# Kernel optimization log

Hardware: AMD Instinct MI355X
Metric: run time of the kernel (lower is better)

The kernel has to match this reference:

```python
import jax, jax.numpy as jnp
import numpy as np
from jax import lax

LEAK = 0.2
GN_EPS = 1e-5
K_NEIGH = 16
GROUPS = 4


def knn_idx(coor_k, coor_q, k):
    # coor_k: [B,Nk,3], coor_q: [B,Nq,3] -> [B,Nq,k] indices of k nearest in coor_k
    d = (jnp.sum(coor_q * coor_q, -1, keepdims=True)
         - 2.0 * jnp.einsum('bqc,bkc->bqk', coor_q, coor_k)
         + jnp.sum(coor_k * coor_k, -1)[:, None, :])
    _, idx = lax.top_k(-d, k)
    return idx


def graph_feature(coor_q, x_q, coor_k, x_k, k):
    # coor_*: [B,3,N*]; x_q: [B,C,Nq]; x_k: [B,C,Nk] -> [B,2C,Nq,k]
    idx = knn_idx(lax.stop_gradient(coor_k).transpose(0, 2, 1),
                  lax.stop_gradient(coor_q).transpose(0, 2, 1), k)
    B = x_k.shape[0]
    x_k_t = x_k.transpose(0, 2, 1)                      # [B,Nk,C]
    b_idx = jnp.arange(B)[:, None, None]
    nb = x_k_t[b_idx, idx]                              # [B,Nq,k,C]
    nb = nb.transpose(0, 3, 1, 2)                       # [B,C,Nq,k]
    xq = x_q[:, :, :, None]                             # [B,C,Nq,1]
    return jnp.concatenate([nb - xq, jnp.broadcast_to(xq, nb.shape)], axis=1)


def conv_gn_lrelu_max(f, w, gamma, beta):
    # f: [B,Cin,N,k]; w: [Cout,Cin] -> [B,Cout,N] (max over k)
    y = jnp.einsum('oc,bcnk->bonk', w, f)
    B, C, N, Kk = y.shape
    g = y.reshape(B, GROUPS, C // GROUPS, N, Kk)
    mu = g.mean((2, 3, 4), keepdims=True)
    var = g.var((2, 3, 4), keepdims=True)
    g = (g - mu) * lax.rsqrt(var + GN_EPS)
    y = g.reshape(B, C, N, Kk) * gamma[None, :, None, None] + beta[None, :, None, None]
    y = jnp.where(y >= 0, y, LEAK * y)
    return y.max(axis=-1)


def fps(xyz, n):
    # xyz: [B,N,3] -> [B,n] int32 (furthest point sampling, start at index 0)
    B, N, _ = xyz.shape
    d0 = jnp.sum((xyz - xyz[:, :1]) ** 2, -1)           # dist to point 0
    def body(dist, _):
        idx = jnp.argmax(dist, -1)                       # [B]
        nxt = jnp.take_along_axis(xyz, idx[:, None, None], 1)
        dist = jnp.minimum(dist, jnp.sum((xyz - nxt) ** 2, -1))
        return dist, idx
    _, idxs = lax.scan(body, d0, None, length=n - 1)     # [n-1,B]
    first = jnp.zeros((1, B), idxs.dtype)
    return jnp.concatenate([first, idxs], 0).T           # [B,n]


def fps_downsample(coor, x, n):
    # coor: [B,3,N], x: [B,C,N] -> ([B,3,n], [B,C,n])
    idx = fps(lax.stop_gradient(coor).transpose(0, 2, 1), n)
    comb = jnp.concatenate([coor, x], axis=1)            # [B,3+C,N]
    b_idx = jnp.arange(coor.shape[0])[:, None]
    new = comb.transpose(0, 2, 1)[b_idx, idx].transpose(0, 2, 1)
    return new[:, :3], new[:, 3:]


def setup_inputs() -> dict:
    key = jax.random.key(0)
    ks = jax.random.split(key, 16)
    s = 0.1
    return {
        'x': jax.random.normal(ks[0], (32, 2048, 3), jnp.float32),
        'w_in': jax.random.normal(ks[1], (8, 3), jnp.float32) * s,
        'b_in': jnp.zeros((8,), jnp.float32),
        'w1': jax.random.normal(ks[2], (32, 16), jnp.float32) * s,
        'g1': jnp.ones((32,), jnp.float32), 'be1': jnp.zeros((32,), jnp.float32),
        'w2': jax.random.normal(ks[3], (64, 64), jnp.float32) * s,
        'g2': jnp.ones((64,), jnp.float32), 'be2': jnp.zeros((64,), jnp.float32),
        'w3': jax.random.normal(ks[4], (64, 128), jnp.float32) * s,
        'g3': jnp.ones((64,), jnp.float32), 'be3': jnp.zeros((64,), jnp.float32),
        'w4': jax.random.normal(ks[5], (256, 128), jnp.float32) * s,
        'g4': jnp.ones((256,), jnp.float32), 'be4': jnp.zeros((256,), jnp.float32),
        'num0': 512,
        'num1': 128,
    }


def reference(x, w_in, b_in, w1, g1, be1, w2, g2, be2, w3, g3, be3, w4, g4, be4, num0, num1):
    coor = x.transpose(0, 2, 1)                          # [B,3,N]
    f = jnp.einsum('oc,bcn->bon', w_in, coor) + b_in[None, :, None]  # input_trans
    f = graph_feature(coor, f, coor, f, K_NEIGH)         # [B,16,N,k]
    f = conv_gn_lrelu_max(f, w1, g1, be1)                # [B,32,N]
    coor_q, f_q = fps_downsample(coor, f, num0)
    f = graph_feature(coor_q, f_q, coor, f, K_NEIGH)     # [B,64,num0,k]
    f = conv_gn_lrelu_max(f, w2, g2, be2)                # [B,64,num0]
    coor = coor_q
    f = graph_feature(coor, f, coor, f, K_NEIGH)         # [B,128,num0,k]
    f = conv_gn_lrelu_max(f, w3, g3, be3)                # [B,64,num0]
    coor_q, f_q = fps_downsample(coor, f, num1)
    f = graph_feature(coor_q, f_q, coor, f, K_NEIGH)     # [B,128,num1,k]
    f = conv_gn_lrelu_max(f, w4, g4, be4)                # [B,256,num1]
    coor = coor_q
    return coor.transpose(0, 2, 1), f.transpose(0, 2, 1)  # [B,num1,3], [B,num1,256]
```

## Files before the change

### kernel.cpp

```cpp
#include <hip/hip_runtime.h>

#define BB 32
#define NPTS0 2048
#define KNB 16
#define KC 256

constexpr int ilog2c(int n){ int l=0; while(n>1){ n>>=1; ++l; } return l; }

static __device__ __forceinline__ float sq3(float a, float b, float c){
  return __fadd_rn(__fadd_rn(__fmul_rn(a,a),__fmul_rn(b,b)),__fmul_rn(c,c));
}

template<int CTRL, int RM>
static __device__ __forceinline__ float dpp_maxf(float v){
  int s = __builtin_amdgcn_update_dpp(__float_as_int(v), __float_as_int(v), CTRL, RM, 0xF, false);
  return fmaxf(v, __int_as_float(s));
}
template<int CTRL, int RM>
static __device__ __forceinline__ unsigned dpp_minu(unsigned v){
  unsigned s = (unsigned)__builtin_amdgcn_update_dpp((int)v, (int)v, CTRL, RM, 0xF, false);
  return s < v ? s : v;
}

static __device__ __forceinline__ void proj_body(const float* __restrict__ x,
    const float* __restrict__ w, const float* __restrict__ bias, float* __restrict__ f0,
    int blk)
{
  int gid = blk*256 + threadIdx.x;
  if (gid >= BB*NPTS0) return;
  float x0 = x[gid*3+0], x1 = x[gid*3+1], x2 = x[gid*3+2];
  #pragma unroll
  for (int o = 0; o < 8; ++o){
    float acc = __fmul_rn(w[o*3+0], x0);
    acc = __fmaf_rn(w[o*3+1], x1, acc);
    acc = __fmaf_rn(w[o*3+2], x2, acc);
    f0[gid*8+o] = __fadd_rn(acc, bias[o]);
  }
}

#define KDECL(I) float th##I = __builtin_inff(); int ti##I = 0;
#define KINS(I,J) if (th##I < th##J){ float tv=th##I; th##I=th##J; th##J=tv; \
                                      int tj=ti##I; ti##I=ti##J; ti##J=tj; }
#define KCASCADE KINS(15,14) KINS(14,13) KINS(13,12) KINS(12,11) KINS(11,10) \
  KINS(10,9) KINS(9,8) KINS(8,7) KINS(7,6) KINS(6,5) KINS(5,4) KINS(4,3) \
  KINS(3,2) KINS(2,1) KINS(1,0)
#define KALLDECL KDECL(0) KDECL(1) KDECL(2) KDECL(3) KDECL(4) KDECL(5) KDECL(6) KDECL(7) \
  KDECL(8) KDECL(9) KDECL(10) KDECL(11) KDECL(12) KDECL(13) KDECL(14) KDECL(15)
#define KST(I) pd[base+I] = th##I; pi[base+I] = (unsigned char)ti##I;
#define KST16(I) pd[base+I] = th##I; pi[base+I] = (unsigned short)ti##I;
#define MST(I) oidx[obase+I] = ti##I;

static __device__ __forceinline__ void knn_part512_body(const float* __restrict__ qpts,
    const float* __restrict__ kpts, int Nq, int Nk, int nkc,
    float* __restrict__ pd, unsigned short* __restrict__ pi,
    int b, int qcb, int kc, float4* kk4)
{
  int tid = threadIdx.x;
  int q = qcb*256 + tid;
  float qx = qpts[(b*Nq+q)*3+0], qy = qpts[(b*Nq+q)*3+1], qz = qpts[(b*Nq+q)*3+2];
  float qq = sq3(qx,qy,qz);
  KALLDECL
  #pragma unroll
  for (int half=0; half<2; ++half){
    __syncthreads();
    {
      int j = kc*512 + half*256 + tid;
      float a = kpts[(b*Nk+j)*3+0];
      float c = kpts[(b*Nk+j)*3+1];
      float dd = kpts[(b*Nk+j)*3+2];
      kk4[tid] = make_float4(a, c, dd, sq3(a,c,dd));
    }
    __syncthreads();
    for (int j=0;j<KC;j++){
      float4 k4 = kk4[j];
      float dot = __fmul_rn(qx,k4.x);
      dot = __fmaf_rn(qy,k4.y,dot);
      dot = __fmaf_rn(qz,k4.z,dot);
      float d = __fadd_rn(__fsub_rn(qq, __fmul_rn(2.0f,dot)), k4.w);
      if (d < th15){
        th15 = d; ti15 = half*256 + j;
        KCASCADE
      }
    }
  }
  size_t base = ((size_t)(b*Nq+q)*nkc + kc)*KNB;
  KST16(0) KST16(1) KST16(2) KST16(3) KST16(4) KST16(5) KST16(6) KST16(7)
  KST16(8) KST16(9) KST16(10) KST16(11) KST16(12) KST16(13) KST16(14) KST16(15)
}

static __device__ __forceinline__ void knn_part_body(const float* __restrict__ qpts,
    const float* __restrict__ kpts, int Nq, int Nk, int nkc,
    float* __restrict__ pd, unsigned char* __restrict__ pi,
    int b, int qcb, int kc, float4* kk4, const int* __restrict__ qidx, int NinQ)
{
  int tid = threadIdx.x;
  {
    int j = kc*KC + tid;
    float a = kpts[(b*Nk+j)*3+0];
    float c = kpts[(b*Nk+j)*3+1];
    float d = kpts[(b*Nk+j)*3+2];
    kk4[tid] = make_float4(a, c, d, sq3(a,c,d));
  }
  __syncthreads();
  int q = qcb*256 + tid;
  if (q >= Nq) return;
  int qrow = qidx ? (b*NinQ + qidx[b*Nq+q]) : (b*Nq+q);
  float qx = qpts[qrow*3+0], qy = qpts[qrow*3+1], qz = qpts[qrow*3+2];
  float qq = sq3(qx,qy,qz);
  KALLDECL
  for (int j=0;j<KC;j++){
    float4 k4 = kk4[j];
    float dot = __fmul_rn(qx,k4.x);
    dot = __fmaf_rn(qy,k4.y,dot);
    dot = __fmaf_rn(qz,k4.z,dot);
    float d = __fadd_rn(__fsub_rn(qq, __fmul_rn(2.0f,dot)), k4.w);
    if (d < th15){
      th15 = d; ti15 = j;
      KCASCADE
    }
  }
  size_t base = ((size_t)(b*Nq+q)*nkc + kc)*KNB;
  KST(0) KST(1) KST(2) KST(3) KST(4) KST(5) KST(6) KST(7)
  KST(8) KST(9) KST(10) KST(11) KST(12) KST(13) KST(14) KST(15)
}

static __device__ __forceinline__ void knn_merge_body(const float* __restrict__ pd,
    const unsigned char* __restrict__ pi, int Nq, int nkc, int* __restrict__ oidx,
    int blk)
{
  int gid = blk*256 + threadIdx.x;
  if (gid >= BB*Nq) return;
  KALLDECL
  size_t base = (size_t)gid*nkc*KNB;
  for (int kc=0;kc<nkc;kc++){
    size_t cb = base + (size_t)kc*KNB;
    for (int i=0;i<KNB;i++){
      float d = pd[cb+i];
      if (d >= th15) break;
      int j = kc*KC + (int)pi[cb+i];
      th15 = d; ti15 = j;
      KCASCADE
    }
  }
  int obase = gid*KNB;
  MST(0) MST(1) MST(2) MST(3) MST(4) MST(5) MST(6) MST(7)
  MST(8) MST(9) MST(10) MST(11) MST(12) MST(13) MST(14) MST(15)
}

static __device__ __forceinline__ void knn_merge512_body(const float* __restrict__ pd,
    const unsigned short* __restrict__ pi, int Nq, int nkc, int* __restrict__ oidx,
    int blk)
{
  int gid = blk*256 + threadIdx.x;
  if (gid >= BB*Nq) return;
  KALLDECL
  size_t base = (size_t)gid*nkc*KNB;
  for (int kc=0;kc<nkc;kc++){
    size_t cb = base + (size_t)kc*KNB;
    for (int i=0;i<KNB;i++){
      float d = pd[cb+i];
      if (d >= th15) break;
      int j = kc*512 + (int)pi[cb+i];
      th15 = d; ti15 = j;
      KCASCADE
    }
  }
  int obase = gid*KNB;
  MST(0) MST(1) MST(2) MST(3) MST(4) MST(5) MST(6) MST(7)
  MST(8) MST(9) MST(10) MST(11) MST(12) MST(13) MST(14) MST(15)
}

#define FPS_LOAD(T) float px##T, py##T, pz##T, d##T; { int i_=T*256+tid; \
  px##T=P[i_*3+0]; py##T=P[i_*3+1]; pz##T=P[i_*3+2]; \
  float dx_=__fsub_rn(px##T,c0x), dy_=__fsub_rn(py##T,c0y), dz_=__fsub_rn(pz##T,c0z); \
  d##T=sq3(dx_,dy_,dz_); bm=fmaxf(bm,d##T); }
#define FPS_MATCH(T) if (d##T == m_w) ci = (unsigned)(T*256 + tid);
#define FPS_OWN(T) if ((idx_w>>8) == T##u){ cx=px##T; cy=py##T; cz=pz##T; }
#define FPS_UPD(T) { float dx_=__fsub_rn(px##T,sx), dy_=__fsub_rn(py##T,sy), dz_=__fsub_rn(pz##T,sz); \
  float nd_=sq3(dx_,dy_,dz_); d##T=fminf(d##T,nd_); nbm=fmaxf(nbm,d##T); }

#define FPS_REDUCE_AND_PICK \
    float v = bm; \
    v = dpp_maxf<0x111, 0xF>(v); \
    v = dpp_maxf<0x112, 0xF>(v); \
    v = dpp_maxf<0x114, 0xF>(v); \
    v = dpp_maxf<0x118, 0xF>(v); \
    v = dpp_maxf<0x142, 0xA>(v); \
    v = dpp_maxf<0x143, 0xC>(v); \
    float m_w = __int_as_float(__builtin_amdgcn_readlane(__float_as_int(v), 63)); \
    unsigned ci = 0xFFFFFFFFu;

#define FPS_MIN_AND_MERGE \
    ci = dpp_minu<0x111, 0xF>(ci); \
    ci = dpp_minu<0x112, 0xF>(ci); \
    ci = dpp_minu<0x114, 0xF>(ci); \
    ci = dpp_minu<0x118, 0xF>(ci); \
    ci = dpp_minu<0x142, 0xA>(ci); \
    ci = dpp_minu<0x143, 0xC>(ci); \
    unsigned idx_w = (unsigned)__builtin_amdgcn_readlane((int)ci, 63); \
    int par = s & 1;

#define FPS_CROSSWAVE \
    __syncthreads(); \
    float4 q0 = *(const float4*)&swp[par][0][0]; float z0 = swp[par][0][4]; \
    float4 q1 = *(const float4*)&swp[par][1][0]; float z1 = swp[par][1][4]; \
    float4 q2 = *(const float4*)&swp[par][2][0]; float z2 = swp[par][2][4]; \
    float4 q3 = *(const float4*)&swp[par][3][0]; float z3 = swp[par][3][4]; \
    float mm = q0.x; unsigned mi = __float_as_uint(q0.y); \
    float sx = q0.z, sy = q0.w, sz = z0; \
    if (q1.x > mm || (q1.x == mm && __float_as_uint(q1.y) < mi)){ \
      mm = q1.x; mi = __float_as_uint(q1.y); sx = q1.z; sy = q1.w; sz = z1; } \
    if (q2.x > mm || (q2.x == mm && __float_as_uint(q2.y) < mi)){ \
      mm = q2.x; mi = __float_as_uint(q2.y); sx = q2.z; sy = q2.w; sz = z2; } \
    if (q3.x > mm || (q3.x == mm && __float_as_uint(q3.y) < mi)){ \
      mm = q3.x; mi = __float_as_uint(q3.y); sx = q3.z; sy = q3.w; sz = z3; } \
    if (tid == 0) oibuf[s] = (int)mi;

static __device__ __forceinline__ void fps8_body(const float* __restrict__ pts,
    int S, int* __restrict__ oidx, int b, char* smraw)
{
  float (*swp)[4][8] = reinterpret_cast<float(*)[4][8]>(smraw);
  int* oibuf = reinterpret_cast<int*>(smraw + 256);
  int tid = threadIdx.x, wid = tid >> 6;
  const float* P = pts + (size_t)b*2048*3;
  float c0x = P[0], c0y = P[1], c0z = P[2];
  float bm = -1.0f;
  FPS_LOAD(0) FPS_LOAD(1) FPS_LOAD(2) FPS_LOAD(3)
  FPS_LOAD(4) FPS_LOAD(5) FPS_LOAD(6) FPS_LOAD(7)
  if (tid == 0) oibuf[0] = 0;
  for (int s=1; s<S; ++s){
    FPS_REDUCE_AND_PICK
    FPS_MATCH(7) FPS_MATCH(6) FPS_MATCH(5) FPS_MATCH(4)
    FPS_MATCH(3) FPS_MATCH(2) FPS_MATCH(1) FPS_MATCH(0)
    FPS_MIN_AND_MERGE
    if (tid == (int)(idx_w & 255u)){
      float cx = px0, cy = py0, cz = pz0;
      FPS_OWN(1) FPS_OWN(2) FPS_OWN(3) FPS_OWN(4) FPS_OWN(5) FPS_OWN(6) FPS_OWN(7)
      float4* wp = (float4*)&swp[par][wid][0];
      *wp = make_float4(m_w, __uint_as_float(idx_w), cx, cy);
      swp[par][wid][4] = cz;
    }
    FPS_CROSSWAVE
    float nbm = -1.0f;
    FPS_UPD(0) FPS_UPD(1) FPS_UPD(2) FPS_UPD(3)
    FPS_UPD(4) FPS_UPD(5) FPS_UPD(6) FPS_UPD(7)
    bm = nbm;
  }
  __syncthreads();
  for (int s2 = tid; s2 < S; s2 += 256) oidx[b*S + s2] = oibuf[s2];
}

static __device__ __forceinline__ void fps2_body(const float* __restrict__ pts,
    int S, int* __restrict__ oidx, int b, char* smraw)
{
  float (*swp)[4][8] = reinterpret_cast<float(*)[4][8]>(smraw);
  int* oibuf = reinterpret_cast<int*>(smraw + 256);
  int tid = threadIdx.x, wid = tid >> 6;
  const float* P = pts + (size_t)b*512*3;
  float c0x = P[0], c0y = P[1], c0z = P[2];
  float bm = -1.0f;
  FPS_LOAD(0) FPS_LOAD(1)
  if (tid == 0) oibuf[0] = 0;
  for (int s=1; s<S; ++s){
    FPS_REDUCE_AND_PICK
    FPS_MATCH(1) FPS_MATCH(0)
    FPS_MIN_AND_MERGE
    if (tid == (int)(idx_w & 255u)){
      float cx = px0, cy = py0, cz = pz0;
      FPS_OWN(1)
      float4* wp = (float4*)&swp[par][wid][0];
      *wp = make_float4(m_w, __uint_as_float(idx_w), cx, cy);
      swp[par][wid][4] = cz;
    }
    FPS_CROSSWAVE
    float nbm = -1.0f;
    FPS_UPD(0) FPS_UPD(1)
    bm = nbm;
  }
  __syncthreads();
  for (int s2 = tid; s2 < S; s2 += 256) oidx[b*S + s2] = oibuf[s2];
}

template<int C, int O, bool DIFF>
static __device__ __forceinline__ void gemv_body(const float* __restrict__ fin,
    const float* __restrict__ W, float* __restrict__ out, int Npts, int blk)
{
  constexpr int NT = O/8;
  constexpr int LNT = ilog2c(NT);
  int gid = blk*256 + threadIdx.x;
  if (gid >= BB*Npts*NT) return;
  int tile = gid & (NT-1);
  int pn = gid >> LNT;
  const float* frow = fin + (size_t)pn*C;
  float f[C];
  #pragma unroll
  for (int c=0;c<C;c++) f[c] = frow[c];
  float acc[8];
  const float* wbase = W + (tile*8)*(2*C);
  #pragma unroll
  for (int oo=0;oo<8;oo++){
    const float* wrow = wbase + oo*(2*C);
    float a = 0.f;
    #pragma unroll
    for (int c=0;c<C;c++){
      float wv = DIFF ? __fsub_rn(wrow[C+c], wrow[c]) : wrow[c];
      a = __fmaf_rn(wv, f[c], a);
    }
    acc[oo] = a;
  }
  float* orow = out + (size_t)pn*O + tile*8;
  #pragma unroll
  for (int oo=0;oo<8;oo++) orow[oo] = acc[oo];
}

template<int C, int O, int LNB>
static __device__ __forceinline__ void gemv_bodyBind(const float* __restrict__ fin,
    const float* __restrict__ W, float* __restrict__ out, int blk,
    const int* __restrict__ gidx, int NinB)
{
  constexpr int NT = O/8;
  constexpr int LNT = ilog2c(NT);
  int gid = blk*256 + threadIdx.x;
  if (gid >= BB*(1<<LNB)*NT) return;
  int tile = gid & (NT-1);
  int pn = gid >> LNT;
  int b = pn >> LNB;
  int src = gidx[pn];
  const float* frow = fin + (size_t)(b*NinB + src)*C;
  float f[C];
  #pragma unroll
  for (int c=0;c<C;c++) f[c] = frow[c];
  float acc[8];
  const float* wbase = W + (tile*8)*(2*C);
  #pragma unroll
  for (int oo=0;oo<8;oo++){
    const float* wrow = wbase + oo*(2*C);
    float a = 0.f;
    #pragma unroll
    for (int c=0;c<C;c++){
      float wv = __fsub_rn(wrow[C+c], wrow[c]);
      a = __fmaf_rn(wv, f[c], a);
    }
    acc[oo] = a;
  }
  float* orow = out + (size_t)pn*O + tile*8;
  #pragma unroll
  for (int oo=0;oo<8;oo++) orow[oo] = acc[oo];
}

template<int C, int O, int LNB, bool BIND>
__global__ __launch_bounds__(256) void gemv_dual_kernel(const float* __restrict__ finA,
    const float* __restrict__ finB, const float* __restrict__ W,
    float* __restrict__ outA, float* __restrict__ outB,
    int NptsA, int NptsB, int nAblk, const int* __restrict__ gidxB, int NinB)
{
  int bid = blockIdx.x;
  if (bid < nAblk) gemv_body<C,O,false>(finA, W, outA, NptsA, bid);
  else if constexpr (BIND) gemv_bodyBind<C,O,LNB>(finB, W, outB, bid-nAblk, gidxB, NinB);
  else gemv_body<C,O,true>(finB, W, outB, NptsB, bid-nAblk);
}

template<int O>
static __device__ __forceinline__ void statsmm_body(const float* __restrict__ A,
    const float* __restrict__ Bq, const int* __restrict__ idx, int Nq, int Nk,
    double* __restrict__ part, float* __restrict__ ymax, float* __restrict__ ymin,
    int b, int split, int nsplit, double* sh )
{
  constexpr int NCH = O/4;
  constexpr int LNCH = ilog2c(NCH);
  constexpr int W = NCH/4;
  int qlen = Nq / nsplit, q0 = split*qlen;
  int tid = threadIdx.x;
  int items = qlen * NCH;
  double s1 = 0.0, s2 = 0.0;
  for (int p = tid; p < items; p += 256){
    int q = q0 + (p >> LNCH);
    int ch = p & (NCH-1);
    const int* ip = idx + (b*Nq+q)*KNB;
    size_t yo = (size_t)(b*Nq+q)*O + ch*4;
    float4 b4 = *(const float4*)(Bq + yo);
    float mx0=-__builtin_inff(), mx1=mx0, mx2=mx0, mx3=mx0;
    float mn0= __builtin_inff(), mn1=mn0, mn2=mn0, mn3=mn0;
    float cs1 = 0.f, cs2 = 0.f;
    #pragma unroll
    for (int kk=0; kk<KNB; ++kk){
      int j = ip[kk];
      float4 a4 = *(const float4*)(A + (size_t)(b*Nk+j)*O + ch*4);
      float y0 = a4.x+b4.x, y1 = a4.y+b4.y, y2 = a4.z+b4.z, y3 = a4.w+b4.w;
      cs1 += ((y0+y1)+(y2+y3));
      cs2 = fmaf(y0,y0,cs2); cs2 = fmaf(y1,y1,cs2);
      cs2 = fmaf(y2,y2,cs2); cs2 = fmaf(y3,y3,cs2);
      mx0=fmaxf(mx0,y0); mx1=fmaxf(mx1,y1); mx2=fmaxf(mx2,y2); mx3=fmaxf(mx3,y3);
      mn0=fminf(mn0,y0); mn1=fminf(mn1,y1); mn2=fminf(mn2,y2); mn3=fminf(mn3,y3);
    }
    *(float4*)(ymax + yo) = make_float4(mx0,mx1,mx2,mx3);
    *(float4*)(ymin + yo) = make_float4(mn0,mn1,mn2,mn3);
    s1 += (double)cs1;
    s2 += (double)cs2;
  }
  if constexpr (W >= 2){ s1 += __shfl_xor(s1,1);  s2 += __shfl_xor(s2,1);  }
  if constexpr (W >= 4){ s1 += __shfl_xor(s1,2);  s2 += __shfl_xor(s2,2);  }
  if constexpr (W >= 8){ s1 += __shfl_xor(s1,4);  s2 += __shfl_xor(s2,4);  }
  if constexpr (W >= 16){ s1 += __shfl_xor(s1,8); s2 += __shfl_xor(s2,8);  }
  if constexpr (NCH <= 8){  s1 += __shfl_xor(s1,8);  s2 += __shfl_xor(s2,8);  }
  if constexpr (NCH <= 16){ s1 += __shfl_xor(s1,16); s2 += __shfl_xor(s2,16); }
  if constexpr (NCH <= 32){ s1 += __shfl_xor(s1,32); s2 += __shfl_xor(s2,32); }
  int lane = tid & 63, wv = tid >> 6;
  if (lane < NCH && (lane & (W-1)) == 0){
    int g = lane / W;
    sh[wv*8+g*2] = s1; sh[wv*8+g*2+1] = s2;
  }
  __syncthreads();
  if (tid == 0){
    #pragma unroll
    for (int g=0; g<4; ++g){
      double t1 = (sh[0*8+g*2]+sh[1*8+g*2]) + (sh[2*8+g*2]+sh[3*8+g*2]);
      double t2 = (sh[0*8+g*2+1]+sh[1*8+g*2+1]) + (sh[2*8+g*2+1]+sh[3*8+g*2+1]);
      int pi = (b*4+g)*nsplit + split;
      part[pi*2] = t1; part[pi*2+1] = t2;
    }
  }
}

template<int O>
__global__ __launch_bounds__(256) void statsmm_kernel(const float* __restrict__ A,
    const float* __restrict__ Bq, const int* __restrict__ idx, int Nq, int Nk,
    double* __restrict__ part, float* __restrict__ ymax, float* __restrict__ ymin)
{
  __shared__ double sh[32];
  statsmm_body<O>(A, Bq, idx, Nq, Nk, part, ymax, ymin,
                  blockIdx.x, blockIdx.y, gridDim.y, sh);
}

template<int O>
__global__ __launch_bounds__(256) void final_kernel(
    const float* __restrict__ ymax, const float* __restrict__ ymin,
    const double* __restrict__ part, int nsplit, double cnt,
    const float* __restrict__ gamma, const float* __restrict__ beta,
    float* __restrict__ fout, int Nq)
{
  constexpr int LO = ilog2c(O);
  constexpr int LO4 = ilog2c(O/4);
  __shared__ float smu[4], srs[4];
  int b = blockIdx.y;
  if (threadIdx.x < 4){
    int g = threadIdx.x;
    int t0 = b*4+g;
    double s1=0.0, s2=0.0;
    for (int i=0;i<nsplit;i++){ s1 += part[(t0*nsplit+i)*2]; s2 += part[(t0*nsplit+i)*2+1]; }
    double mean = s1/cnt;
    double var = s2/cnt - mean*mean;
    double rstd = 1.0 / sqrt(var + 1e-5);
    smu[g] = (float)mean;
    srs[g] = (float)rstd;
  }
  __syncthreads();
  int t = blockIdx.x*256 + threadIdx.x;
  if (t >= Nq*O) return;
  int o = t & (O-1);
  int q = t >> LO;
  int g = o >> LO4;
  float gam = gamma[o], bet = beta[o];
  size_t yo = (size_t)(b*Nq+q)*O + o;
  float ysel = (gam >= 0.f) ? ymax[yo] : ymin[yo];
  float yn = __fmul_rn(__fsub_rn(ysel, smu[g]), srs[g]);
  float yv = __fadd_rn(__fmul_rn(yn, gam), bet);
  fout[yo] = yv >= 0.f ? yv : 0.2f*yv;
}

static __device__ __forceinline__ void gatherc_body(const int* __restrict__ fidx,
    const float* __restrict__ pts, float* __restrict__ cq, int Nin, int Nout, int blk)
{
  int gid = blk*256 + threadIdx.x;
  if (gid >= BB*Nout) return;
  int b = gid / Nout;
  int i = gid - b*Nout;
  int src = fidx[b*Nout + i];
  #pragma unroll
  for (int c=0;c<3;c++) cq[gid*3+c] = pts[(b*Nin+src)*3+c];
}

__global__ __launch_bounds__(256) void gatherc_kernel(const int* __restrict__ fidx,
    const float* __restrict__ pts, float* __restrict__ cq, int Nin, int Nout)
{
  gatherc_body(fidx, pts, cq, Nin, Nout, blockIdx.x);
}

__global__ __launch_bounds__(256) void fused1_kernel(const float* __restrict__ x,
    const float* __restrict__ w_in, const float* __restrict__ b_in,
    float* __restrict__ f0, float* __restrict__ pd1, unsigned short* __restrict__ pi1,
    int* __restrict__ fidx0)
{
  __shared__ __align__(16) char sm[4096];
  int bid = blockIdx.x;
  if (bid < 32){
    __builtin_amdgcn_s_setprio(3);
    fps8_body(x, 512, fidx0, bid, sm);
  } else if (bid < 32+1024){
    int r = bid - 32;
    int b = r & 31; int rest = r >> 5;
    knn_part512_body(x, x, 2048, 2048, 4, pd1, pi1, b, rest & 7, rest >> 3, (float4*)sm);
  } else {
    proj_body(x, w_in, b_in, f0, bid - 1056);
  }
}

__global__ __launch_bounds__(256) void fused2_kernel(const float* __restrict__ coorq1,
    const float* __restrict__ x,
    float* __restrict__ pd2, unsigned char* __restrict__ pi2,
    float* __restrict__ pd3, unsigned char* __restrict__ pi3,
    int* __restrict__ fidx1,
    const float* __restrict__ pd1, const unsigned short* __restrict__ pi1,
    int* __restrict__ idx1,
    const float* __restrict__ f0, const float* __restrict__ w1,
    float* __restrict__ A1, float* __restrict__ B1)
{
  __shared__ __align__(16) char sm[4096];
  int bid = blockIdx.x;
  if (bid < 32){
    __builtin_amdgcn_s_setprio(3);
    fps2_body(coorq1, 128, fidx1, bid, sm);
  } else if (bid < 32+512){
    int r = bid - 32;
    int b = r & 31; int rest = r >> 5;
    knn_part_body(coorq1, x, 512, 2048, 8, pd2, pi2, b, rest & 1, rest >> 1,
                  (float4*)sm, nullptr, 0);
  } else if (bid < 32+512+128){
    int r = bid - 544;
    int b = r & 31; int rest = r >> 5;
    knn_part_body(coorq1, coorq1, 512, 512, 2, pd3, pi3, b, rest & 1, rest >> 1,
                  (float4*)sm, nullptr, 0);
  } else if (bid < 928){
    knn_merge512_body(pd1, pi1, 2048, 4, idx1, bid - 672);
  } else if (bid < 1952){
    gemv_body<8,32,false>(f0, w1, A1, 2048, bid - 928);
  } else {
    gemv_body<8,32,true>(f0, w1, B1, 2048, bid - 1952);
  }
}

__global__ __launch_bounds__(256) void fused3_kernel(
    const float* __restrict__ A1, const float* __restrict__ B1,
    const int* __restrict__ idx1, double* __restrict__ part,
    float* __restrict__ ymax, float* __restrict__ ymin,
    const float* __restrict__ pd2, const unsigned char* __restrict__ pi2, int* __restrict__ idx2,
    const float* __restrict__ pd3, const unsigned char* __restrict__ pi3, int* __restrict__ idx3,
    const float* __restrict__ coorq1, const int* __restrict__ fidx1,
    float* __restrict__ pd4, unsigned char* __restrict__ pi4,
    float* __restrict__ coor_out)
{
  __shared__ __align__(16) char sm[4096];
  int bid = blockIdx.x;
  if (bid < 256){
    statsmm_body<32>(A1, B1, idx1, 2048, 2048, part, ymax, ymin,
                     bid >> 3, bid & 7, 8, (double*)sm);
  } else if (bid < 320){
    knn_merge_body(pd2, pi2, 512, 8, idx2, bid - 256);
  } else if (bid < 384){
    knn_merge_body(pd3, pi3, 512, 2, idx3, bid - 320);
  } else if (bid < 448){
    int r = bid - 384;
    int b = r & 31; int kc = r >> 5;
    knn_part_body(coorq1, coorq1, 128, 512, 2, pd4, pi4, b, 0, kc,
                  (float4*)sm, fidx1, 512);
  } else {
    gatherc_body(fidx1, coorq1, coor_out, 512, 128, bid - 448);
  }
}

__global__ __launch_bounds__(256) void fused4_kernel(const float* __restrict__ f1,
    const float* __restrict__ w2, float* __restrict__ A, float* __restrict__ Bq,
    const int* __restrict__ fidx0,
    const float* __restrict__ pd4, const unsigned char* __restrict__ pi4,
    int* __restrict__ idx4)
{
  int bid = blockIdx.x;
  if (bid < 2048) gemv_body<32,64,false>(f1, w2, A, 2048, bid);
  else if (bid < 2560) gemv_bodyBind<32,64,9>(f1, w2, Bq, bid - 2048, fidx0, 2048);
  else knn_merge_body(pd4, pi4, 128, 2, idx4, bid - 2560);
}

extern "C" void kernel_launch(void* const* d_in, const int* in_sizes, int n_in,
                              void* d_out, int out_size, void* d_ws, size_t ws_size,
                              hipStream_t stream)
{
  (void)in_sizes; (void)n_in; (void)out_size; (void)ws_size;
  const float* x    = (const float*)d_in[0];
  const float* w_in = (const float*)d_in[1];
  const float* b_in = (const float*)d_in[2];
  const float* w1 = (const float*)d_in[3];
  const float* g1 = (const float*)d_in[4];
  const float* be1= (const float*)d_in[5];
  const float* w2 = (const float*)d_in[6];
  const float* g2 = (const float*)d_in[7];
  const float* be2= (const float*)d_in[8];
  const float* w3 = (const float*)d_in[9];
  const float* g3 = (const float*)d_in[10];
  const float* be3= (const float*)d_in[11];
  const float* w4 = (const float*)d_in[12];
  const float* g4 = (const float*)d_in[13];
  const float* be4= (const float*)d_in[14];

  float* out = (float*)d_out;
  float* coor_out = out;
  float* f_out = out + BB*128*3;

  char* ws = (char*)d_ws;
  size_t off = 0;
  auto alloc = [&](size_t bytes)->void*{ void* p = ws + off; off += (bytes + 255) & ~(size_t)255; return p; };

  float* f0     = (float*)alloc((size_t)BB*2048*8*4);
  int*   idx1   = (int*)  alloc((size_t)BB*2048*16*4);
  float* f1     = (float*)alloc((size_t)BB*2048*32*4);
  double* part  = (double*)alloc((size_t)BB*4*8*2*8);
  int*   fidx0  = (int*)  alloc((size_t)BB*512*4);
  float* coorq1 = (float*)alloc((size_t)BB*512*3*4);
  int*   idx2   = (int*)  alloc((size_t)BB*512*16*4);
  float* f2     = (float*)alloc((size_t)BB*512*64*4);
  int*   idx3   = (int*)  alloc((size_t)BB*512*16*4);
  float* f3     = (float*)alloc((size_t)BB*512*64*4);
  int*   fidx1  = (int*)  alloc((size_t)BB*128*4);
  int*   idx4   = (int*)  alloc((size_t)BB*128*16*4);
  float* pd2          = (float*)alloc((size_t)BB*512*8*KNB*4);
  unsigned char* pi2  = (unsigned char*)alloc((size_t)BB*512*8*KNB);
  float* pd3          = (float*)alloc((size_t)BB*512*2*KNB*4);
  unsigned char* pi3  = (unsigned char*)alloc((size_t)BB*512*2*KNB);
  float* pd4          = (float*)alloc((size_t)BB*128*2*KNB*4);
  unsigned char* pi4  = (unsigned char*)alloc((size_t)BB*128*2*KNB);

  char* U = (char*)alloc((size_t)40<<20);
  float* pd1          = (float*)U;
  unsigned short* pi1 = (unsigned short*)(U + ((size_t)16<<20));
  float* A1 = (float*)(U + ((size_t)24<<20));
  float* B1 = (float*)(U + ((size_t)32<<20));
  float* ymax = (float*)U;
  float* ymin = (float*)(U + ((size_t)8<<20));
  float* A  = (float*)(U + ((size_t)16<<20));
  float* Bq = (float*)(U + ((size_t)32<<20));

  auto cdiv = [](int a, int b){ return (a+b-1)/b; };

  fused1_kernel<<<1312,256,0,stream>>>(x, w_in, b_in, f0, pd1, pi1, fidx0);
  gatherc_kernel<<<cdiv(BB*512,256),256,0,stream>>>(fidx0, x, coorq1, 2048, 512);
  fused2_kernel<<<2976,256,0,stream>>>(coorq1, x, pd2, pi2, pd3, pi3, fidx1,
                                       pd1, pi1, idx1, f0, w1, A1, B1);
  fused3_kernel<<<464,256,0,stream>>>(A1, B1, idx1, part, ymax, ymin,
                                      pd2, pi2, idx2, pd3, pi3, idx3,
                                      coorq1, fidx1, pd4, pi4, coor_out);
  final_kernel<32><<<dim3(cdiv(2048*32,256),BB),256,0,stream>>>(ymax, ymin, part, 8,
      8.0*2048*16, g1, be1, f1, 2048);
  fused4_kernel<<<2576,256,0,stream>>>(f1, w2, A, Bq, fidx0, pd4, pi4, idx4);
  statsmm_kernel<64><<<dim3(BB,8),256,0,stream>>>(A, Bq, idx2, 512, 2048, part, ymax, ymin);
  final_kernel<64><<<dim3(cdiv(512*64,256),BB),256,0,stream>>>(ymax, ymin, part, 8,
      16.0*512*16, g2, be2, f2, 512);
  gemv_dual_kernel<64,64,0,false><<<1024,256,0,stream>>>(f2, f2, w3, A, Bq,
      512, 512, 512, nullptr, 0);
  statsmm_kernel<64><<<dim3(BB,8),256,0,stream>>>(A, Bq, idx3, 512, 512, part, ymax, ymin);
  final_kernel<64><<<dim3(cdiv(512*64,256),BB),256,0,stream>>>(ymax, ymin, part, 8,
      16.0*512*16, g3, be3, f3, 512);
  gemv_dual_kernel<64,256,7,true><<<2560,256,0,stream>>>(f3, f3, w4, A, Bq,
      512, 128, 2048, fidx1, 512);
  statsmm_kernel<256><<<dim3(BB,8),256,0,stream>>>(A, Bq, idx4, 128, 512, part, ymax, ymin);
  final_kernel<256><<<dim3(cdiv(128*256,256),BB),256,0,stream>>>(ymax, ymin, part, 8,
      64.0*128*16, g4, be4, f_out, 128);
}
```

Baseline: 1.196 ms.

## Split first FPS across two fused kernels with checkpointed distances and regroup stages

```diff
diff --git a/kernel.cpp b/kernel.cpp
--- a/kernel.cpp
+++ b/kernel.cpp
@@ -4,6 +4,7 @@
 #define NPTS0 2048
 #define KNB 16
 #define KC 256
+#define FSPLIT 257
 
 constexpr int ilog2c(int n){ int l=0; while(n>1){ n>>=1; ++l; } return l; }
 
@@ -174,6 +175,10 @@
   px##T=P[i_*3+0]; py##T=P[i_*3+1]; pz##T=P[i_*3+2]; \
   float dx_=__fsub_rn(px##T,c0x), dy_=__fsub_rn(py##T,c0y), dz_=__fsub_rn(pz##T,c0z); \
   d##T=sq3(dx_,dy_,dz_); bm=fmaxf(bm,d##T); }
+#define FPS_RELOAD(T) float px##T, py##T, pz##T, d##T; { int i_=T*256+tid; \
+  px##T=P[i_*3+0]; py##T=P[i_*3+1]; pz##T=P[i_*3+2]; \
+  d##T = ckpt[(size_t)b*2048 + i_]; bm=fmaxf(bm,d##T); }
+#define FPS_SAVE(T) { int i_=T*256+tid; ckpt[(size_t)b*2048 + i_] = d##T; }
 #define FPS_MATCH(T) if (d##T == m_w) ci = (unsigned)(T*256 + tid);
 #define FPS_OWN(T) if ((idx_w>>8) == T##u){ cx=px##T; cy=py##T; cz=pz##T; }
 #define FPS_UPD(T) { float dx_=__fsub_rn(px##T,sx), dy_=__fsub_rn(py##T,sy), dz_=__fsub_rn(pz##T,sz); \
@@ -200,7 +205,7 @@
     unsigned idx_w = (unsigned)__builtin_amdgcn_readlane((int)ci, 63); \
     int par = s & 1;
 
-#define FPS_CROSSWAVE \
+#define FPS_CROSSWAVE(OIDXEXPR) \
     __syncthreads(); \
     float4 q0 = *(const float4*)&swp[par][0][0]; float z0 = swp[par][0][4]; \
     float4 q1 = *(const float4*)&swp[par][1][0]; float z1 = swp[par][1][4]; \
@@ -214,10 +219,28 @@
       mm = q2.x; mi = __float_as_uint(q2.y); sx = q2.z; sy = q2.w; sz = z2; } \
     if (q3.x > mm || (q3.x == mm && __float_as_uint(q3.y) < mi)){ \
       mm = q3.x; mi = __float_as_uint(q3.y); sx = q3.z; sy = q3.w; sz = z3; } \
-    if (tid == 0) oibuf[s] = (int)mi;
-
-static __device__ __forceinline__ void fps8_body(const float* __restrict__ pts,
-    int S, int* __restrict__ oidx, int b, char* smraw)
+    if (tid == 0) oibuf[OIDXEXPR] = (int)mi;
+
+#define FPS8_ITER(OIDXEXPR) \
+    FPS_REDUCE_AND_PICK \
+    FPS_MATCH(7) FPS_MATCH(6) FPS_MATCH(5) FPS_MATCH(4) \
+    FPS_MATCH(3) FPS_MATCH(2) FPS_MATCH(1) FPS_MATCH(0) \
+    FPS_MIN_AND_MERGE \
+    if (tid == (int)(idx_w & 255u)){ \
+      float cx = px0, cy = py0, cz = pz0; \
+      FPS_OWN(1) FPS_OWN(2) FPS_OWN(3) FPS_OWN(4) FPS_OWN(5) FPS_OWN(6) FPS_OWN(7) \
+      float4* wp = (float4*)&swp[par][wid][0]; \
+      *wp = make_float4(m_w, __uint_as_float(idx_w), cx, cy); \
+      swp[par][wid][4] = cz; \
+    } \
+    FPS_CROSSWAVE(OIDXEXPR) \
+    float nbm = -1.0f; \
+    FPS_UPD(0) FPS_UPD(1) FPS_UPD(2) FPS_UPD(3) \
+    FPS_UPD(4) FPS_UPD(5) FPS_UPD(6) FPS_UPD(7) \
+    bm = nbm;
+
+static __device__ __forceinline__ void fps8a_body(const float* __restrict__ pts,
+    int* __restrict__ oidx, float* __restrict__ ckpt, int b, char* smraw)
 {
   float (*swp)[4][8] = reinterpret_cast<float(*)[4][8]>(smraw);
   int* oibuf = reinterpret_cast<int*>(smraw + 256);
@@ -228,26 +251,30 @@
   FPS_LOAD(0) FPS_LOAD(1) FPS_LOAD(2) FPS_LOAD(3)
   FPS_LOAD(4) FPS_LOAD(5) FPS_LOAD(6) FPS_LOAD(7)
   if (tid == 0) oibuf[0] = 0;
-  for (int s=1; s<S; ++s){
-    FPS_REDUCE_AND_PICK
-    FPS_MATCH(7) FPS_MATCH(6) FPS_MATCH(5) FPS_MATCH(4)
-    FPS_MATCH(3) FPS_MATCH(2) FPS_MATCH(1) FPS_MATCH(0)
-    FPS_MIN_AND_MERGE
-    if (tid == (int)(idx_w & 255u)){
-      float cx = px0, cy = py0, cz = pz0;
-      FPS_OWN(1) FPS_OWN(2) FPS_OWN(3) FPS_OWN(4) FPS_OWN(5) FPS_OWN(6) FPS_OWN(7)
-      float4* wp = (float4*)&swp[par][wid][0];
-      *wp = make_float4(m_w, __uint_as_float(idx_w), cx, cy);
-      swp[par][wid][4] = cz;
-    }
-    FPS_CROSSWAVE
-    float nbm = -1.0f;
-    FPS_UPD(0) FPS_UPD(1) FPS_UPD(2) FPS_UPD(3)
-    FPS_UPD(4) FPS_UPD(5) FPS_UPD(6) FPS_UPD(7)
-    bm = nbm;
-  }
+  for (int s=1; s<FSPLIT; ++s){
+    FPS8_ITER(s)
+  }
+  FPS_SAVE(0) FPS_SAVE(1) FPS_SAVE(2) FPS_SAVE(3)
+  FPS_SAVE(4) FPS_SAVE(5) FPS_SAVE(6) FPS_SAVE(7)
   __syncthreads();
-  for (int s2 = tid; s2 < S; s2 += 256) oidx[b*S + s2] = oibuf[s2];
+  for (int s2 = tid; s2 < FSPLIT; s2 += 256) oidx[b*512 + s2] = oibuf[s2];
+}
+
+static __device__ __forceinline__ void fps8b_body(const float* __restrict__ pts,
+    int* __restrict__ oidx, const float* __restrict__ ckpt, int b, char* smraw)
+{
+  float (*swp)[4][8] = reinterpret_cast<float(*)[4][8]>(smraw);
+  int* oibuf = reinterpret_cast<int*>(smraw + 256);
+  int tid = threadIdx.x, wid = tid >> 6;
+  const float* P = pts + (size_t)b*2048*3;
+  float bm = -1.0f;
+  FPS_RELOAD(0) FPS_RELOAD(1) FPS_RELOAD(2) FPS_RELOAD(3)
+  FPS_RELOAD(4) FPS_RELOAD(5) FPS_RELOAD(6) FPS_RELOAD(7)
+  for (int s=FSPLIT; s<512; ++s){
+    FPS8_ITER(s - FSPLIT)
+  }
+  __syncthreads();
+  for (int s2 = tid; s2 < 512-FSPLIT; s2 += 256) oidx[b*512 + FSPLIT + s2] = oibuf[s2];
 }
 
 static __device__ __forceinline__ void fps2_body(const float* __restrict__ pts,
@@ -272,7 +299,7 @@
       *wp = make_float4(m_w, __uint_as_float(idx_w), cx, cy);
       swp[par][wid][4] = cz;
     }
-    FPS_CROSSWAVE
+    FPS_CROSSWAVE(s)
     float nbm = -1.0f;
     FPS_UPD(0) FPS_UPD(1)
     bm = nbm;
@@ -433,16 +460,14 @@
 }
 
 template<int O>
-__global__ __launch_bounds__(256) void final_kernel(
+static __device__ __forceinline__ void final_body(
     const float* __restrict__ ymax, const float* __restrict__ ymin,
     const double* __restrict__ part, int nsplit, double cnt,
     const float* __restrict__ gamma, const float* __restrict__ beta,
-    float* __restrict__ fout, int Nq)
+    float* __restrict__ fout, int Nq, int xblk, int b, float* smu, float* srs)
 {
   constexpr int LO = ilog2c(O);
   constexpr int LO4 = ilog2c(O/4);
-  __shared__ float smu[4], srs[4];
-  int b = blockIdx.y;
   if (threadIdx.x < 4){
     int g = threadIdx.x;
     int t0 = b*4+g;
@@ -455,7 +480,7 @@
     srs[g] = (float)rstd;
   }
   __syncthreads();
-  int t = blockIdx.x*256 + threadIdx.x;
+  int t = xblk*256 + threadIdx.x;
   if (t >= Nq*O) return;
   int o = t & (O-1);
   int q = t >> LO;
@@ -468,6 +493,18 @@
   fout[yo] = yv >= 0.f ? yv : 0.2f*yv;
 }
 
+template<int O>
+__global__ __launch_bounds__(256) void final_kernel(
+    const float* __restrict__ ymax, const float* __restrict__ ymin,
+    const double* __restrict__ part, int nsplit, double cnt,
+    const float* __restrict__ gamma, const float* __restrict__ beta,
+    float* __restrict__ fout, int Nq)
+{
+  __shared__ float smu[4], srs[4];
+  final_body<O>(ymax, ymin, part, nsplit, cnt, gamma, beta, fout, Nq,
+                blockIdx.x, blockIdx.y, smu, srs);
+}
+
 static __device__ __forceinline__ void gatherc_body(const int* __restrict__ fidx,
     const float* __restrict__ pts, float* __restrict__ cq, int Nin, int Nout, int blk)
 {
@@ -489,13 +526,13 @@
 __global__ __launch_bounds__(256) void fused1_kernel(const float* __restrict__ x,
     const float* __restrict__ w_in, const float* __restrict__ b_in,
     float* __restrict__ f0, float* __restrict__ pd1, unsigned short* __restrict__ pi1,
-    int* __restrict__ fidx0)
+    int* __restrict__ fidx0, float* __restrict__ fpsckpt)
 {
   __shared__ __align__(16) char sm[4096];
   int bid = blockIdx.x;
   if (bid < 32){
     __builtin_amdgcn_s_setprio(3);
-    fps8_body(x, 512, fidx0, bid, sm);
+    fps8a_body(x, fidx0, fpsckpt, bid, sm);
   } else if (bid < 32+1024){
     int r = bid - 32;
     int b = r & 31; int rest = r >> 5;
@@ -505,44 +542,63 @@
   }
 }
 
-__global__ __launch_bounds__(256) void fused2_kernel(const float* __restrict__ coorq1,
-    const float* __restrict__ x,
-    float* __restrict__ pd2, unsigned char* __restrict__ pi2,
-    float* __restrict__ pd3, unsigned char* __restrict__ pi3,
-    int* __restrict__ fidx1,
+__global__ __launch_bounds__(256) void fused2_kernel(const float* __restrict__ x,
+    int* __restrict__ fidx0, const float* __restrict__ fpsckpt,
     const float* __restrict__ pd1, const unsigned short* __restrict__ pi1,
     int* __restrict__ idx1,
     const float* __restrict__ f0, const float* __restrict__ w1,
     float* __restrict__ A1, float* __restrict__ B1)
+{
+  __shared__ __align__(16) char sm[4096];
+  int bid = blockIdx.x;
+  if (bid < 32){
+    __builtin_amdgcn_s_setprio(3);
+    fps8b_body(x, fidx0, fpsckpt, bid, sm);
+  } else if (bid < 32+256){
+    knn_merge512_body(pd1, pi1, 2048, 4, idx1, bid - 32);
+  } else if (bid < 32+256+1024){
+    gemv_body<8,32,false>(f0, w1, A1, 2048, bid - 288);
+  } else {
+    gemv_body<8,32,true>(f0, w1, B1, 2048, bid - 1312);
+  }
+}
+
+__global__ __launch_bounds__(256) void fused3_kernel(const float* __restrict__ coorq1,
+    const float* __restrict__ x,
+    int* __restrict__ fidx1,
+    const float* __restrict__ A1, const float* __restrict__ B1,
+    const int* __restrict__ idx1, double* __restrict__ part,
+    float* __restrict__ ymax, float* __restrict__ ymin,
+    float* __restrict__ pd2, unsigned char* __restrict__ pi2,
+    float* __restrict__ pd3, unsigned char* __restrict__ pi3)
 {
   __shared__ __align__(16) char sm[4096];
   int bid = blockIdx.x;
   if (bid < 32){
     __builtin_amdgcn_s_setprio(3);
     fps2_body(coorq1, 128, fidx1, bid, sm);
-  } else if (bid < 32+512){
+  } else if (bid < 32+256){
     int r = bid - 32;
+    statsmm_body<32>(A1, B1, idx1, 2048, 2048, part, ymax, ymin,
+                     r >> 3, r & 7, 8, (double*)sm);
+  } else if (bid < 32+256+512){
+    int r = bid - 288;
     int b = r & 31; int rest = r >> 5;
     knn_part_body(coorq1, x, 512, 2048, 8, pd2, pi2, b, rest & 1, rest >> 1,
                   (float4*)sm, nullptr, 0);
-  } else if (bid < 32+512+128){
-    int r = bid - 544;
+  } else {
+    int r = bid - 800;
     int b = r & 31; int rest = r >> 5;
     knn_part_body(coorq1, coorq1, 512, 512, 2, pd3, pi3, b, rest & 1, rest >> 1,
                   (float4*)sm, nullptr, 0);
-  } else if (bid < 928){
-    knn_merge512_body(pd1, pi1, 2048, 4, idx1, bid - 672);
-  } else if (bid < 1952){
-    gemv_body<8,32,false>(f0, w1, A1, 2048, bid - 928);
-  } else {
-    gemv_body<8,32,true>(f0, w1, B1, 2048, bid - 1952);
-  }
-}
-
-__global__ __launch_bounds__(256) void fused3_kernel(
-    const float* __restrict__ A1, const float* __restrict__ B1,
-    const int* __restrict__ idx1, double* __restrict__ part,
-    float* __restrict__ ymax, float* __restrict__ ymin,
+  }
+}
+
+__global__ __launch_bounds__(256) void fused4_kernel(
+    const float* __restrict__ ymax, const float* __restrict__ ymin,
+    const double* __restrict__ part,
+    const float* __restrict__ g1, const float* __restrict__ be1,
+    float* __restrict__ f1,
     const float* __restrict__ pd2, const unsigned char* __restrict__ pi2, int* __restrict__ idx2,
     const float* __restrict__ pd3, const unsigned char* __restrict__ pi3, int* __restrict__ idx3,
     const float* __restrict__ coorq1, const int* __restrict__ fidx1,
@@ -551,24 +607,26 @@
 {
   __shared__ __align__(16) char sm[4096];
   int bid = blockIdx.x;
-  if (bid < 256){
-    statsmm_body<32>(A1, B1, idx1, 2048, 2048, part, ymax, ymin,
-                     bid >> 3, bid & 7, 8, (double*)sm);
-  } else if (bid < 320){
-    knn_merge_body(pd2, pi2, 512, 8, idx2, bid - 256);
-  } else if (bid < 384){
-    knn_merge_body(pd3, pi3, 512, 2, idx3, bid - 320);
-  } else if (bid < 448){
-    int r = bid - 384;
+  if (bid < 8192){
+    float* smu = (float*)sm;
+    float* srs = (float*)(sm + 16);
+    final_body<32>(ymax, ymin, part, 8, 8.0*2048*16, g1, be1, f1, 2048,
+                   bid & 255, bid >> 8, smu, srs);
+  } else if (bid < 8256){
+    knn_merge_body(pd2, pi2, 512, 8, idx2, bid - 8192);
+  } else if (bid < 8320){
+    knn_merge_body(pd3, pi3, 512, 2, idx3, bid - 8256);
+  } else if (bid < 8384){
+    int r = bid - 8320;
     int b = r & 31; int kc = r >> 5;
     knn_part_body(coorq1, coorq1, 128, 512, 2, pd4, pi4, b, 0, kc,
                   (float4*)sm, fidx1, 512);
   } else {
-    gatherc_body(fidx1, coorq1, coor_out, 512, 128, bid - 448);
-  }
-}
-
-__global__ __launch_bounds__(256) void fused4_kernel(const float* __restrict__ f1,
+    gatherc_body(fidx1, coorq1, coor_out, 512, 128, bid - 8384);
+  }
+}
+
+__global__ __launch_bounds__(256) void fused5_kernel(const float* __restrict__ f1,
     const float* __restrict__ w2, float* __restrict__ A, float* __restrict__ Bq,
     const int* __restrict__ fidx0,
     const float* __restrict__ pd4, const unsigned char* __restrict__ pi4,
@@ -621,6 +679,7 @@
   float* f3     = (float*)alloc((size_t)BB*512*64*4);
   int*   fidx1  = (int*)  alloc((size_t)BB*128*4);
   int*   idx4   = (int*)  alloc((size_t)BB*128*16*4);
+  float* fpsckpt = (float*)alloc((size_t)BB*2048*4);
   float* pd2          = (float*)alloc((size_t)BB*512*8*KNB*4);
   unsigned char* pi2  = (unsigned char*)alloc((size_t)BB*512*8*KNB);
   float* pd3          = (float*)alloc((size_t)BB*512*2*KNB*4);
@@ -640,16 +699,15 @@
 
   auto cdiv = [](int a, int b){ return (a+b-1)/b; };
 
-  fused1_kernel<<<1312,256,0,stream>>>(x, w_in, b_in, f0, pd1, pi1, fidx0);
+  fused1_kernel<<<1312,256,0,stream>>>(x, w_in, b_in, f0, pd1, pi1, fidx0, fpsckpt);
+  fused2_kernel<<<2336,256,0,stream>>>(x, fidx0, fpsckpt, pd1, pi1, idx1, f0, w1, A1, B1);
   gatherc_kernel<<<cdiv(BB*512,256),256,0,stream>>>(fidx0, x, coorq1, 2048, 512);
-  fused2_kernel<<<2976,256,0,stream>>>(coorq1, x, pd2, pi2, pd3, pi3, fidx1,
-                                       pd1, pi1, idx1, f0, w1, A1, B1);
-  fused3_kernel<<<464,256,0,stream>>>(A1, B1, idx1, part, ymax, ymin,
-                                      pd2, pi2, idx2, pd3, pi3, idx3,
-                                      coorq1, fidx1, pd4, pi4, coor_out);
-  final_kernel<32><<<dim3(cdiv(2048*32,256),BB),256,0,stream>>>(ymax, ymin, part, 8,
-      8.0*2048*16, g1, be1, f1, 2048);
-  fused4_kernel<<<2576,256,0,stream>>>(f1, w2, A, Bq, fidx0, pd4, pi4, idx4);
+  fused3_kernel<<<928,256,0,stream>>>(coorq1, x, fidx1, A1, B1, idx1, part,
+                                      ymax, ymin, pd2, pi2, pd3, pi3);
+  fused4_kernel<<<8400,256,0,stream>>>(ymax, ymin, part, g1, be1, f1,
+                                       pd2, pi2, idx2, pd3, pi3, idx3,
+                                       coorq1, fidx1, pd4, pi4, coor_out);
+  fused5_kernel<<<2576,256,0,stream>>>(f1, w2, A, Bq, fidx0, pd4, pi4, idx4);
   statsmm_kernel<64><<<dim3(BB,8),256,0,stream>>>(A, Bq, idx2, 512, 2048, part, ymax, ymin);
   final_kernel<64><<<dim3(cdiv(512*64,256),BB),256,0,stream>>>(ymax, ymin, part, 8,
       16.0*512*16, g2, be2, f2, 512);
```

Measured after the change: 1.352 ms. +13.1%, slower.
